# Optimization experiments

Measured on AMD Instinct MI355X. Metric: run time of the kernel, lower is better.

## Reference

```python
import jax, jax.numpy as jnp
import numpy as np

B, N, H, D = 16, 512, 8, 128  # batch, nodes, heads, hid_dim (per-head dim == hid_dim)


def setup_inputs() -> dict:
    key = jax.random.key(0)
    ks = jax.random.split(key, 12)
    x = jax.random.normal(ks[0], (B, N, D), dtype=jnp.float32)
    dist = jax.random.normal(ks[1], (B, N, N), dtype=jnp.float32)
    mask = (jax.random.uniform(ks[2], (B, N)) < 0.9).astype(jnp.float32)
    w_std = 0.02
    Wq = jax.random.normal(ks[3], (D, H * D), dtype=jnp.float32) * w_std
    Wk = jax.random.normal(ks[4], (D, H * D), dtype=jnp.float32) * w_std
    Wv = jax.random.normal(ks[5], (D, H * D), dtype=jnp.float32) * w_std
    Wo = jax.random.normal(ks[6], (H * D, D), dtype=jnp.float32) * w_std
    bq = jax.random.normal(ks[7], (H * D,), dtype=jnp.float32) * w_std
    bk = jax.random.normal(ks[8], (H * D,), dtype=jnp.float32) * w_std
    bv = jax.random.normal(ks[9], (H * D,), dtype=jnp.float32) * w_std
    bo = jax.random.normal(ks[10], (D,), dtype=jnp.float32) * w_std
    return {"x": x, "dist": dist, "mask": mask,
            "Wq": Wq, "bq": bq, "Wk": Wk, "bk": bk,
            "Wv": Wv, "bv": bv, "Wo": Wo, "bo": bo}


def reference(x, dist, mask, Wq, bq, Wk, bk, Wv, bv, Wo, bo):
    scale = jnp.asarray(D, x.dtype) ** -0.5
    # projections: [B,N,H*D] -> [B,H,N,D]
    q = (x @ Wq + bq).reshape(B, N, H, D).transpose(0, 2, 1, 3)
    k = (x @ Wk + bk).reshape(B, N, H, D).transpose(0, 2, 1, 3)
    v = (x @ Wv + bv).reshape(B, N, H, D).transpose(0, 2, 1, 3)
    m = mask[:, None, :, None]  # [B,1,N,1]
    q = q * m * scale
    k = k * m
    v = v * m
    a = jnp.einsum('bhnd,bhmd->bhnm', q, k)  # [B,H,N,N]
    a = a + dist[:, None, :, :]  # dist bias broadcast over heads
    amask = (mask[:, :, None] * mask[:, None, :])[:, None, :, :]  # [B,1,N,N]
    a = jnp.where(amask == 0, jnp.asarray(-1e9, a.dtype), a)
    a = jax.nn.softmax(a, axis=-1)
    a = jnp.where(amask == 0, jnp.asarray(0.0, a.dtype), a)
    y = jnp.einsum('bhnm,bhmd->bhnd', a, v)
    y = y.transpose(0, 2, 1, 3).reshape(B, N, H * D)
    y = y @ Wo + bo
    return y * mask[:, :, None]
```

## Files before the change

### kernel.cpp

```cpp
#include <hip/hip_runtime.h>
#include <hip/hip_bf16.h>

#define B_ 16
#define N_ 512
#define H_ 8
#define D_ 128
#define HD_ 1024
#define SCALE_ 0.08838834764831845f

typedef __attribute__((ext_vector_type(8))) short bf16x8;
typedef __attribute__((ext_vector_type(4))) float f32x4;
typedef __attribute__((ext_vector_type(4))) _Float16 f16x4;

__device__ __forceinline__ unsigned short f2bf(float f) {
    union { __hip_bfloat16 h; unsigned short u; } cv;
    cv.h = __float2bfloat16(f);
    return cv.u;
}
__device__ __forceinline__ unsigned short f2h(float f) {
    union { _Float16 h; unsigned short u; } cv;
    cv.h = (_Float16)f;
    return cv.u;
}

#define BAR_LIGHT() do {                                     \
    asm volatile("s_waitcnt lgkmcnt(0)" ::: "memory");       \
    __builtin_amdgcn_s_barrier();                            \
    asm volatile("" ::: "memory");                           \
} while (0)

__global__ __launch_bounds__(256) void prep_kernel(
    const float* __restrict__ Wq, const float* __restrict__ Wk,
    const float* __restrict__ Wv, const float* __restrict__ Wo,
    unsigned short* __restrict__ wTh, unsigned short* __restrict__ woT)
{
    __shared__ float T[32][33];
    const int tile = blockIdx.x;
    const int t = threadIdx.x;
    if (tile < 384) {
        const int w = tile / 128;
        const int rem = tile % 128;
        const int kt = rem & 3;
        const int ct = rem >> 2;
        const float* W = (w == 0) ? Wq : (w == 1) ? Wk : Wv;
        const int k0 = kt * 32, c0 = ct * 32;
        #pragma unroll
        for (int u = 0; u < 4; u++) {
            int lin = t + 256 * u; int r = lin >> 5, c = lin & 31;
            T[r][c] = W[(size_t)(k0 + r) * 1024 + c0 + c];
        }
        __syncthreads();
        unsigned short* oh = wTh + (size_t)w * 131072;
        #pragma unroll
        for (int u = 0; u < 4; u++) {
            int lin = t + 256 * u; int c = lin >> 5, r = lin & 31;
            oh[(size_t)(c0 + c) * 128 + k0 + r] = f2bf(T[r][c]);
        }
    } else {
        const int rem = tile - 384;
        const int nt = rem & 3;
        const int kt = rem >> 2;
        const int k0 = kt * 32, n0 = nt * 32;
        #pragma unroll
        for (int u = 0; u < 4; u++) {
            int lin = t + 256 * u; int r = lin >> 5, c = lin & 31;
            T[r][c] = Wo[(size_t)(k0 + r) * 128 + n0 + c];
        }
        __syncthreads();
        #pragma unroll
        for (int u = 0; u < 4; u++) {
            int lin = t + 256 * u; int c = lin >> 5, r = lin & 31;
            woT[(size_t)(n0 + c) * 1024 + k0 + r] = f2bf(T[r][c]);
        }
    }
}

__global__ __launch_bounds__(256, 3) void qkv_kernel(
    const float* __restrict__ x, const float* __restrict__ mask,
    const unsigned short* __restrict__ wTh,
    const float* __restrict__ bq, const float* __restrict__ bk,
    const float* __restrict__ bv,
    unsigned short* __restrict__ q, unsigned short* __restrict__ k,
    unsigned short* __restrict__ vT)
{
    const int cb = blockIdx.x % 24;
    const int by = blockIdx.x / 24;
    const int row0 = by * 128, c0 = cb * 128;
    const int which = c0 >> 10, w0 = c0 & 1023;
    const float* bi = (which == 0) ? bq : (which == 1) ? bk : bv;

    __shared__ alignas(16) unsigned short Wh[128][136];
    __shared__ float biS[128];
    __shared__ float mskS[128];

    const int t = threadIdx.x;
    if (t < 128) { biS[t] = bi[w0 + t]; mskS[t] = mask[row0 + t]; }

    const unsigned short* whp = wTh + (size_t)which * 131072 + (size_t)w0 * 128;
    #pragma unroll
    for (int u = 0; u < 8; u++) {
        int lin = t + 256 * u; int c = lin >> 4, k8 = (lin & 15) * 8;
        *(bf16x8*)&Wh[c][k8] = *(const bf16x8*)&whp[(size_t)c * 128 + k8];
    }

    const int wave = t >> 6, lane = t & 63, m16 = lane & 15, g4 = lane >> 4;
    const int rw = row0 + wave * 32;

    bf16x8 ah[2][4];
    #pragma unroll
    for (int mt = 0; mt < 2; mt++)
        #pragma unroll
        for (int kc = 0; kc < 4; kc++) {
            const float* xp = &x[(size_t)(rw + mt * 16 + m16) * 128 + kc * 32 + g4 * 8];
            float4 v0 = *(const float4*)xp;
            float4 v1 = *(const float4*)(xp + 4);
            float vv[8] = {v0.x, v0.y, v0.z, v0.w, v1.x, v1.y, v1.z, v1.w};
            union { bf16x8 v; unsigned short s[8]; } Hh;
            #pragma unroll
            for (int e = 0; e < 8; e++) Hh.s[e] = f2bf(vv[e]);
            ah[mt][kc] = Hh.v;
        }
    __syncthreads();

    const f32x4 zero = {0.f, 0.f, 0.f, 0.f};
    f32x4 acc[2][8];
    #pragma unroll
    for (int mt = 0; mt < 2; mt++)
        #pragma unroll
        for (int nt = 0; nt < 8; nt++) acc[mt][nt] = zero;

    #pragma unroll
    for (int nt = 0; nt < 8; nt++) {
        #pragma unroll
        for (int kc = 0; kc < 4; kc++) {
            bf16x8 bh = *(const bf16x8*)&Wh[nt * 16 + m16][kc * 32 + g4 * 8];
            #pragma unroll
            for (int mt = 0; mt < 2; mt++)
                acc[mt][nt] = __builtin_amdgcn_mfma_f32_16x16x32_bf16(ah[mt][kc], bh, acc[mt][nt], 0, 0, 0);
        }
    }
    __syncthreads();

    const int b = row0 >> 9, h = w0 >> 7;
    const int iseq0 = row0 & 511;
    unsigned short* Tr = &Wh[0][0];

    if (which == 2) {
        #pragma unroll
        for (int mt = 0; mt < 2; mt++)
            #pragma unroll
            for (int nt = 0; nt < 8; nt++)
                #pragma unroll
                for (int r = 0; r < 4; r++) {
                    int rowl = wave * 32 + mt * 16 + g4 * 4 + r;
                    int col = nt * 16 + m16;
                    Tr[col * 136 + rowl] = f2h((acc[mt][nt][r] + biS[col]) * mskS[rowl]);
                }
        __syncthreads();
        unsigned short* vbase = vT + (size_t)(b * 8 + h) * 128 * 512 + iseq0;
        #pragma unroll
        for (int u = 0; u < 8; u++) {
            int lin = t + 256 * u; int dl = lin >> 4, i8 = (lin & 15) * 8;
            *(bf16x8*)&vbase[(size_t)dl * 512 + i8] = *(const bf16x8*)&Tr[dl * 136 + i8];
        }
    } else {
        const float sc = (which == 0) ? SCALE_ : 1.0f;
        #pragma unroll
        for (int mt = 0; mt < 2; mt++)
            #pragma unroll
            for (int nt = 0; nt < 8; nt++)
                #pragma unroll
                for (int r = 0; r < 4; r++) {
                    int rowl = wave * 32 + mt * 16 + g4 * 4 + r;
                    int col = nt * 16 + m16;
                    Tr[rowl * 136 + col] = f2bf((acc[mt][nt][r] + biS[col]) * (mskS[rowl] * sc));
                }
        __syncthreads();
        unsigned short* dst = ((which == 0) ? q : k) +
                              ((size_t)(b * 8 + h) * 512 + iseq0) * 128;
        #pragma unroll
        for (int u = 0; u < 8; u++) {
            int lin = t + 256 * u; int rl = lin >> 4, c8 = (lin & 15) * 8;
            *(bf16x8*)&dst[(size_t)rl * 128 + c8] = *(const bf16x8*)&Tr[rl * 136 + c8];
        }
    }
}

__global__ __launch_bounds__(256, 2) void attn_kernel(
    const unsigned short* __restrict__ q, const unsigned short* __restrict__ k,
    const unsigned short* __restrict__ vT, const float* __restrict__ dist,
    const float* __restrict__ mask, unsigned short* __restrict__ y)
{
    const int xid = blockIdx.x;
    const int b = (xid & 7) | ((xid >> 8) << 3);
    const int itile = (xid >> 3) & 3;
    const int h = (xid >> 5) & 7;
    const int bh = b * 8 + h;
    const int i0 = itile * 128;

    const unsigned short* qb = q + (size_t)bh * 512 * 128;
    const unsigned short* kb = k + (size_t)bh * 512 * 128;
    const unsigned short* vb = vT + (size_t)bh * 128 * 512;

    __shared__ alignas(16) unsigned short Ks[2][64][136];
    __shared__ alignas(16) unsigned short Vs[2][128][76];
    __shared__ alignas(16) float cmS[512];

    const int t = threadIdx.x;
    const int wave = t >> 6, lane = t & 63;
    const int m16 = lane & 15, g4 = lane >> 4;
    const int iw = i0 + wave * 32;

    cmS[t] = (mask[b * 512 + t] == 0.0f) ? -1e9f : 0.0f;
    cmS[256 + t] = (mask[b * 512 + 256 + t] == 0.0f) ? -1e9f : 0.0f;

    bf16x8 aq0[4], aq1[4];
    #pragma unroll
    for (int c = 0; c < 4; c++) {
        aq0[c] = *(const bf16x8*)(qb + (size_t)(iw + m16) * 128 + c * 32 + g4 * 8);
        aq1[c] = *(const bf16x8*)(qb + (size_t)(iw + 16 + m16) * 128 + c * 32 + g4 * 8);
    }

    const int krow = t >> 2, kcol = (t & 3) * 32;
    const int vrow = t >> 1, vcol = (t & 1) * 32;

    const float* dbase = dist + ((size_t)b * 512 + iw) * 512;

    bf16x8 kp[4], vp[4];
    #pragma unroll
    for (int u = 0; u < 4; u++) {
        kp[u] = *(const bf16x8*)(kb + (size_t)krow * 128 + kcol + u * 8);
        vp[u] = *(const bf16x8*)(vb + (size_t)vrow * 512 + vcol + u * 8);
    }
    #pragma unroll
    for (int u = 0; u < 4; u++) {
        *(bf16x8*)&Ks[0][krow][kcol + u * 8] = kp[u];
        union { bf16x8 v8; ushort4 h4[2]; } cv; cv.v8 = vp[u];
        *(ushort4*)&Vs[0][vrow][vcol + u * 8] = cv.h4[0];
        *(ushort4*)&Vs[0][vrow][vcol + u * 8 + 4] = cv.h4[1];
    }
    BAR_LIGHT();

    const f32x4 zero = {0.f, 0.f, 0.f, 0.f};
    float rl0 = 0.f, rl1 = 0.f;
    f32x4 Ot0[8] = {zero, zero, zero, zero, zero, zero, zero, zero};
    f32x4 Ot1[8] = {zero, zero, zero, zero, zero, zero, zero, zero};

    for (int c = 0; c < 8; c++) {
        const int j0 = c * 64;
        const int bsel = c & 1;

        if (c < 7) {
            const int j0n = j0 + 64;
            #pragma unroll
            for (int u = 0; u < 4; u++) {
                kp[u] = *(const bf16x8*)(kb + (size_t)(j0n + krow) * 128 + kcol + u * 8);
                vp[u] = *(const bf16x8*)(vb + (size_t)vrow * 512 + j0n + vcol + u * 8);
            }
        }

        f32x4 dv0[4], dv1[4];
        #pragma unroll
        for (int jt = 0; jt < 4; jt++) {
            dv0[jt] = *(const f32x4*)&dbase[(size_t)m16 * 512 + j0 + jt * 16 + g4 * 4];
            dv1[jt] = *(const f32x4*)&dbase[(size_t)(16 + m16) * 512 + j0 + jt * 16 + g4 * 4];
        }

        f32x4 s0[4], s1[4];
        #pragma unroll
        for (int jt = 0; jt < 4; jt++) {
            f32x4 a0 = zero, a1 = zero;
            #pragma unroll
            for (int cc = 0; cc < 4; cc++) {
                bf16x8 kf = *(const bf16x8*)&Ks[bsel][jt * 16 + m16][cc * 32 + g4 * 8];
                a0 = __builtin_amdgcn_mfma_f32_16x16x32_bf16(kf, aq0[cc], a0, 0, 0, 0);
                a1 = __builtin_amdgcn_mfma_f32_16x16x32_bf16(kf, aq1[cc], a1, 0, 0, 0);
            }
            s0[jt] = a0; s1[jt] = a1;
        }

        f16x4 pa0[4], pa1[4];
        float ps0 = 0.f, ps1 = 0.f;
        #pragma unroll
        for (int jt = 0; jt < 4; jt++) {
            f32x4 cm4 = *(const f32x4*)&cmS[j0 + jt * 16 + g4 * 4];
            #pragma unroll
            for (int r = 0; r < 4; r++) {
                float p0 = __expf(s0[jt][r] + dv0[jt][r] + cm4[r]);
                float p1 = __expf(s1[jt][r] + dv1[jt][r] + cm4[r]);
                ps0 += p0; ps1 += p1;
                pa0[jt][r] = (_Float16)p0;
                pa1[jt][r] = (_Float16)p1;
            }
        }
        rl0 += ps0; rl1 += ps1;

        if (c < 7) {
            const int bo = bsel ^ 1;
            #pragma unroll
            for (int u = 0; u < 4; u++) {
                *(bf16x8*)&Ks[bo][krow][kcol + u * 8] = kp[u];
                union { bf16x8 v8; ushort4 h4[2]; } cv; cv.v8 = vp[u];
                *(ushort4*)&Vs[bo][vrow][vcol + u * 8] = cv.h4[0];
                *(ushort4*)&Vs[bo][vrow][vcol + u * 8 + 4] = cv.h4[1];
            }
        }

        #pragma unroll
        for (int jt = 0; jt < 4; jt++)
            #pragma unroll
            for (int dt = 0; dt < 8; dt++) {
                f16x4 vf = *(const f16x4*)&Vs[bsel][dt * 16 + m16][jt * 16 + g4 * 4];
                Ot0[dt] = __builtin_amdgcn_mfma_f32_16x16x16f16(pa0[jt], vf, Ot0[dt], 0, 0, 0);
                Ot1[dt] = __builtin_amdgcn_mfma_f32_16x16x16f16(pa1[jt], vf, Ot1[dt], 0, 0, 0);
            }

        if (c < 7) BAR_LIGHT();
    }
    BAR_LIGHT();

    rl0 += __shfl_xor(rl0, 16); rl0 += __shfl_xor(rl0, 32);
    rl1 += __shfl_xor(rl1, 16); rl1 += __shfl_xor(rl1, 32);
    float rs0 = (rl0 > 0.f) ? 1.0f / rl0 : 0.f;
    float rs1 = (rl1 > 0.f) ? 1.0f / rl1 : 0.f;
    float rs04[4], rs14[4];
    #pragma unroll
    for (int r = 0; r < 4; r++) {
        rs04[r] = __shfl(rs0, g4 * 4 + r);
        rs14[r] = __shfl(rs1, g4 * 4 + r);
    }
    unsigned short (*Sb)[136] = (wave >> 1) ? Ks[1] : Ks[0];
    const int rb = (wave & 1) * 32;
    #pragma unroll
    for (int dt = 0; dt < 8; dt++)
        #pragma unroll
        for (int r = 0; r < 4; r++) {
            Sb[rb + g4 * 4 + r][dt * 16 + m16]      = f2bf(Ot0[dt][r] * rs04[r]);
            Sb[rb + 16 + g4 * 4 + r][dt * 16 + m16] = f2bf(Ot1[dt][r] * rs14[r]);
        }
    #pragma unroll
    for (int u = 0; u < 8; u++) {
        int lin = lane + 64 * u;
        int row = lin >> 4;
        int seg = lin & 15;
        *(bf16x8*)&y[((size_t)(b * 512) + iw + row) * 1024 + h * 128 + seg * 8] =
            *(const bf16x8*)&Sb[rb + row][seg * 8];
    }
}

__global__ __launch_bounds__(256, 2) void oproj_kernel(
    const unsigned short* __restrict__ Y, const unsigned short* __restrict__ woT,
    const float* __restrict__ bo, const float* __restrict__ mask,
    float* __restrict__ out)
{
    const int row0 = blockIdx.x * 16;
    __shared__ alignas(16) unsigned short Ys[16][136];
    __shared__ alignas(16) unsigned short Ws[128][136];
    __shared__ float boS[128];
    __shared__ float mskS[16];

    const int t = threadIdx.x;
    if (t < 128) boS[t] = bo[t];
    if (t < 16) mskS[t] = mask[row0 + t];

    const int wave = t >> 6, lane = t & 63;
    const int m16 = lane & 15, g4 = lane >> 4;
    const int n0 = wave * 32;

    const int yr = t >> 4, yk = (t & 15) * 8;
    const int wn = t >> 4, wk = (t & 15) * 8;

    const f32x4 zero = {0.f, 0.f, 0.f, 0.f};
    f32x4 acc[2] = {zero, zero};

    bf16x8 yp, wp[8];
    yp = *(const bf16x8*)&Y[(size_t)(row0 + yr) * 1024 + yk];
    #pragma unroll
    for (int u = 0; u < 8; u++)
        wp[u] = *(const bf16x8*)&woT[(size_t)(wn + u * 16) * 1024 + wk];

    for (int c = 0; c < 8; c++) {
        __syncthreads();
        *(bf16x8*)&Ys[yr][yk] = yp;
        #pragma unroll
        for (int u = 0; u < 8; u++) *(bf16x8*)&Ws[wn + u * 16][wk] = wp[u];
        __syncthreads();
        if (c < 7) {
            const int kc0 = (c + 1) * 128;
            yp = *(const bf16x8*)&Y[(size_t)(row0 + yr) * 1024 + kc0 + yk];
            #pragma unroll
            for (int u = 0; u < 8; u++)
                wp[u] = *(const bf16x8*)&woT[(size_t)(wn + u * 16) * 1024 + kc0 + wk];
        }
        #pragma unroll
        for (int kc = 0; kc < 4; kc++) {
            bf16x8 a = *(const bf16x8*)&Ys[m16][kc * 32 + g4 * 8];
            #pragma unroll
            for (int nt = 0; nt < 2; nt++) {
                bf16x8 bb = *(const bf16x8*)&Ws[n0 + nt * 16 + m16][kc * 32 + g4 * 8];
                acc[nt] = __builtin_amdgcn_mfma_f32_16x16x32_bf16(a, bb, acc[nt], 0, 0, 0);
            }
        }
    }
    __syncthreads();

    float* Ot = (float*)&Ws[0][0];
    #pragma unroll
    for (int nt = 0; nt < 2; nt++)
        #pragma unroll
        for (int r = 0; r < 4; r++) {
            int rowl = g4 * 4 + r;
            int col = n0 + nt * 16 + m16;
            Ot[rowl * 132 + col] = (acc[nt][r] + boS[col]) * mskS[rowl];
        }
    __syncthreads();
    #pragma unroll
    for (int u = 0; u < 2; u++) {
        int lin = t + 256 * u; int r = lin >> 5, c4 = lin & 31;
        *(float4*)&out[(size_t)(row0 + r) * 128 + c4 * 4] =
            *(const float4*)&Ot[r * 132 + c4 * 4];
    }
}

extern "C" void kernel_launch(void* const* d_in, const int* in_sizes, int n_in,
                              void* d_out, int out_size, void* d_ws, size_t ws_size,
                              hipStream_t stream) {
    const float* x    = (const float*)d_in[0];
    const float* dist = (const float*)d_in[1];
    const float* mask = (const float*)d_in[2];
    const float* Wq   = (const float*)d_in[3];
    const float* bq   = (const float*)d_in[4];
    const float* Wk   = (const float*)d_in[5];
    const float* bk   = (const float*)d_in[6];
    const float* Wv   = (const float*)d_in[7];
    const float* bv   = (const float*)d_in[8];
    const float* Wo   = (const float*)d_in[9];
    const float* bo   = (const float*)d_in[10];
    float* out = (float*)d_out;

    const size_t per = (size_t)B_ * H_ * N_ * D_;
    unsigned short* qb  = (unsigned short*)d_ws;
    unsigned short* kb  = qb + per;
    unsigned short* vb  = kb + per;
    unsigned short* yb  = vb + per;
    unsigned short* wTh = yb + per;
    unsigned short* woT = wTh + 3 * 131072;

    prep_kernel<<<512, 256, 0, stream>>>(Wq, Wk, Wv, Wo, wTh, woT);
    qkv_kernel<<<1536, 256, 0, stream>>>(x, mask, wTh, bq, bk, bv, qb, kb, vb);
    attn_kernel<<<512, 256, 0, stream>>>(qb, kb, vb, dist, mask, yb);
    oproj_kernel<<<512, 256, 0, stream>>>(yb, woT, bo, mask, out);
}
```

Measured before the change: 150.3 us.

## Load V fragments directly from global memory instead of staging through LDS

Drops the double-buffered LDS tile for V^T. Each lane now reads its f16x4 V fragments straight from global memory (L2/L1) into registers, in an A/B ping-pong pattern interleaved with the PV MFMAs. This removes the LDS writes and reads for V and shrinks LDS use, at the cost of more global load traffic (each wave re-reads V redundantly) and more VGPR pressure. Global latency may be poorly hidden.

```diff
diff --git a/kernel.cpp b/kernel.cpp
--- a/kernel.cpp
+++ b/kernel.cpp
@@ -203,7 +203,6 @@
     const unsigned short* vb = vT + (size_t)bh * 128 * 512;
 
     __shared__ alignas(16) unsigned short Ks[2][64][136];
-    __shared__ alignas(16) unsigned short Vs[2][128][76];
     __shared__ alignas(16) float cmS[512];
 
     const int t = threadIdx.x;
@@ -222,23 +221,17 @@
     }
 
     const int krow = t >> 2, kcol = (t & 3) * 32;
-    const int vrow = t >> 1, vcol = (t & 1) * 32;
 
     const float* dbase = dist + ((size_t)b * 512 + iw) * 512;
-
-    bf16x8 kp[4], vp[4];
-    #pragma unroll
-    for (int u = 0; u < 4; u++) {
+    const unsigned short* vlane = vb + (size_t)m16 * 512 + g4 * 4;
+
+    bf16x8 kp[4];
+    #pragma unroll
+    for (int u = 0; u < 4; u++)
         kp[u] = *(const bf16x8*)(kb + (size_t)krow * 128 + kcol + u * 8);
-        vp[u] = *(const bf16x8*)(vb + (size_t)vrow * 512 + vcol + u * 8);
-    }
-    #pragma unroll
-    for (int u = 0; u < 4; u++) {
+    #pragma unroll
+    for (int u = 0; u < 4; u++)
         *(bf16x8*)&Ks[0][krow][kcol + u * 8] = kp[u];
-        union { bf16x8 v8; ushort4 h4[2]; } cv; cv.v8 = vp[u];
-        *(ushort4*)&Vs[0][vrow][vcol + u * 8] = cv.h4[0];
-        *(ushort4*)&Vs[0][vrow][vcol + u * 8 + 4] = cv.h4[1];
-    }
     BAR_LIGHT();
 
     const f32x4 zero = {0.f, 0.f, 0.f, 0.f};
@@ -250,20 +243,23 @@
         const int j0 = c * 64;
         const int bsel = c & 1;
 
-        if (c < 7) {
-            const int j0n = j0 + 64;
-            #pragma unroll
-            for (int u = 0; u < 4; u++) {
-                kp[u] = *(const bf16x8*)(kb + (size_t)(j0n + krow) * 128 + kcol + u * 8);
-                vp[u] = *(const bf16x8*)(vb + (size_t)vrow * 512 + j0n + vcol + u * 8);
-            }
-        }
+        f16x4 vfA[8], vfB[8];
+        #pragma unroll
+        for (int dt = 0; dt < 8; dt++)
+            vfA[dt] = *(const f16x4*)(vlane + (size_t)dt * 16 * 512 + j0);
 
         f32x4 dv0[4], dv1[4];
         #pragma unroll
         for (int jt = 0; jt < 4; jt++) {
             dv0[jt] = *(const f32x4*)&dbase[(size_t)m16 * 512 + j0 + jt * 16 + g4 * 4];
             dv1[jt] = *(const f32x4*)&dbase[(size_t)(16 + m16) * 512 + j0 + jt * 16 + g4 * 4];
+        }
+
+        if (c < 7) {
+            const int j0n = j0 + 64;
+            #pragma unroll
+            for (int u = 0; u < 4; u++)
+                kp[u] = *(const bf16x8*)(kb + (size_t)(j0n + krow) * 128 + kcol + u * 8);
         }
 
         f32x4 s0[4], s1[4];
@@ -278,6 +274,10 @@
             }
             s0[jt] = a0; s1[jt] = a1;
         }
+
+        #pragma unroll
+        for (int dt = 0; dt < 8; dt++)
+            vfB[dt] = *(const f16x4*)(vlane + (size_t)dt * 16 * 512 + j0 + 16);
 
         f16x4 pa0[4], pa1[4];
         float ps0 = 0.f, ps1 = 0.f;
@@ -298,22 +298,36 @@
         if (c < 7) {
             const int bo = bsel ^ 1;
             #pragma unroll
-            for (int u = 0; u < 4; u++) {
+            for (int u = 0; u < 4; u++)
                 *(bf16x8*)&Ks[bo][krow][kcol + u * 8] = kp[u];
-                union { bf16x8 v8; ushort4 h4[2]; } cv; cv.v8 = vp[u];
-                *(ushort4*)&Vs[bo][vrow][vcol + u * 8] = cv.h4[0];
-                *(ushort4*)&Vs[bo][vrow][vcol + u * 8 + 4] = cv.h4[1];
-            }
-        }
-
-        #pragma unroll
-        for (int jt = 0; jt < 4; jt++)
-            #pragma unroll
-            for (int dt = 0; dt < 8; dt++) {
-                f16x4 vf = *(const f16x4*)&Vs[bsel][dt * 16 + m16][jt * 16 + g4 * 4];
-                Ot0[dt] = __builtin_amdgcn_mfma_f32_16x16x16f16(pa0[jt], vf, Ot0[dt], 0, 0, 0);
-                Ot1[dt] = __builtin_amdgcn_mfma_f32_16x16x16f16(pa1[jt], vf, Ot1[dt], 0, 0, 0);
-            }
+        }
+
+        #pragma unroll
+        for (int dt = 0; dt < 8; dt++) {
+            Ot0[dt] = __builtin_amdgcn_mfma_f32_16x16x16f16(pa0[0], vfA[dt], Ot0[dt], 0, 0, 0);
+            Ot1[dt] = __builtin_amdgcn_mfma_f32_16x16x16f16(pa1[0], vfA[dt], Ot1[dt], 0, 0, 0);
+        }
+        #pragma unroll
+        for (int dt = 0; dt < 8; dt++)
+            vfA[dt] = *(const f16x4*)(vlane + (size_t)dt * 16 * 512 + j0 + 32);
+        #pragma unroll
+        for (int dt = 0; dt < 8; dt++) {
+            Ot0[dt] = __builtin_amdgcn_mfma_f32_16x16x16f16(pa0[1], vfB[dt], Ot0[dt], 0, 0, 0);
+            Ot1[dt] = __builtin_amdgcn_mfma_f32_16x16x16f16(pa1[1], vfB[dt], Ot1[dt], 0, 0, 0);
+        }
+        #pragma unroll
+        for (int dt = 0; dt < 8; dt++)
+            vfB[dt] = *(const f16x4*)(vlane + (size_t)dt * 16 * 512 + j0 + 48);
+        #pragma unroll
+        for (int dt = 0; dt < 8; dt++) {
+            Ot0[dt] = __builtin_amdgcn_mfma_f32_16x16x16f16(pa0[2], vfA[dt], Ot0[dt], 0, 0, 0);
+            Ot1[dt] = __builtin_amdgcn_mfma_f32_16x16x16f16(pa1[2], vfA[dt], Ot1[dt], 0, 0, 0);
+        }
+        #pragma unroll
+        for (int dt = 0; dt < 8; dt++) {
+            Ot0[dt] = __builtin_amdgcn_mfma_f32_16x16x16f16(pa0[3], vfB[dt], Ot0[dt], 0, 0, 0);
+            Ot1[dt] = __builtin_amdgcn_mfma_f32_16x16x16f16(pa1[3], vfB[dt], Ot1[dt], 0, 0, 0);
+        }
 
         if (c < 7) BAR_LIGHT();
     }
```

Measured after the change: 195.4 us. 30.0% more time.
